# Kernel tuning notes

Hardware: AMD Instinct MI355X
Metric: run time of the kernel (lower is better)

The kernel has to match this reference:

```python
import jax, jax.numpy as jnp
import numpy as np

D_MODEL = 2048
M = 128          # compression rate
N_H = 16         # query heads
C = 128          # head dim
D_C = 512        # query compression dim
N_GROUPS = 4
D_G = 512
ROPE_DIM = 64
EPS = 1e-6
B, S = 2, 8192


def _layernorm(x, gamma, beta):
    mu = x.mean(axis=-1, keepdims=True)
    var = ((x - mu) ** 2).mean(axis=-1, keepdims=True)
    return (x - mu) * jax.lax.rsqrt(var + EPS) * gamma + beta


def _partial_rope(q):
    # q: [B,S,H,C]; rotate last ROPE_DIM dims with interleaved complex RoPE
    half = ROPE_DIM // 2
    inv_freq = 1.0 / (10000.0 ** (jnp.arange(0, ROPE_DIM, 2, dtype=jnp.float32) / ROPE_DIM))
    ang = jnp.arange(S, dtype=jnp.float32)[:, None] * inv_freq[None, :]   # [S,half]
    cos = jnp.cos(ang)[None, :, None, :]
    sin = jnp.sin(ang)[None, :, None, :]
    x_part, x_rope = q[..., : C - ROPE_DIM], q[..., C - ROPE_DIM:]
    e, o = x_rope[..., 0::2], x_rope[..., 1::2]
    re = e * cos - o * sin
    ro = e * sin + o * cos
    rot = jnp.stack([re, ro], axis=-1).reshape(*e.shape[:-1], ROPE_DIM)
    return jnp.concatenate([x_part, rot.astype(q.dtype)], axis=-1)


def setup_inputs() -> dict:
    key = jax.random.key(0)
    ks = jax.random.split(key, 12)
    std = 0.02
    inp = {
        "x": jax.random.normal(ks[0], (B, S, D_MODEL), jnp.float32),
        "w_kv": jax.random.normal(ks[1], (D_MODEL, C), jnp.float32) * std,
        "w_z": jax.random.normal(ks[2], (D_MODEL, C), jnp.float32) * std,
        "b_comp": jax.random.normal(ks[3], (M, C), jnp.float32) * std,
        "w_dq": jax.random.normal(ks[4], (D_MODEL, D_C), jnp.float32) * std,
        "w_uq": jax.random.normal(ks[5], (D_C, N_H * C), jnp.float32) * std,
        "o_down_w": jax.random.normal(ks[6], (N_GROUPS, (N_H // N_GROUPS) * C, D_G), jnp.float32) * std,
        "o_up_w": jax.random.normal(ks[7], (N_GROUPS * D_G, D_MODEL), jnp.float32) * std,
        "kv_gamma": jnp.ones((C,), jnp.float32),
        "kv_beta": jnp.zeros((C,), jnp.float32),
        "q_gamma": jnp.ones((C,), jnp.float32),
        "q_beta": jnp.zeros((C,), jnp.float32),
        "sink_logits": jnp.zeros((N_H,), jnp.float32),
    }
    return inp


def reference(x, w_kv, w_z, b_comp, w_dq, w_uq, o_down_w, o_up_w,
              kv_gamma, kv_beta, q_gamma, q_beta, sink_logits):
    n_comp = S // M
    # ---- HeavyCompressor: softmax-weighted pooling per non-overlapping block
    c_proj = x @ w_kv                                     # [B,S,C]
    z = x @ w_z                                           # [B,S,C]
    zb = z.reshape(B, n_comp, M, C) + b_comp              # [B,Nc,M,C]
    w = jax.nn.softmax(zb, axis=2)
    comp = (w * c_proj.reshape(B, n_comp, M, C)).sum(axis=2)   # [B,Nc,C]
    k_comp = _layernorm(comp, kv_gamma, kv_beta)
    v_comp = comp
    # ---- queries: low-rank down/up projection, per-head LN, partial RoPE
    q = (x @ w_dq @ w_uq).reshape(B, S, N_H, C)
    q = _layernorm(q, q_gamma, q_beta)
    q = _partial_rope(q)
    # ---- dense attention over compressed KV with sink-logit denominator
    scores = jnp.einsum("bshc,bkc->bhsk", q.astype(jnp.float32),
                        k_comp.astype(jnp.float32)) / (C ** 0.5)
    allowed = jnp.arange(S)[:, None] >= jnp.arange(n_comp)[None, :] * M  # [S,Nc]
    p = jnp.where(allowed[None, None], jnp.exp(scores), 0.0)
    sink = jnp.exp(sink_logits).reshape(1, N_H, 1, 1)
    attn = p / (p.sum(axis=-1, keepdims=True) + sink)
    out = jnp.einsum("bhsk,bkc->bshc", attn.astype(x.dtype),
                     v_comp.astype(jnp.float32)).astype(x.dtype)
    # ---- grouped output projection
    gsz = N_H // N_GROUPS
    out_g = out.reshape(B, S, N_GROUPS, gsz * C)
    down = jnp.einsum("bsgi,gio->bsgo", out_g, o_down_w).reshape(B, S, N_GROUPS * D_G)
    return down @ o_up_w                                  # [B,S,D_MODEL]
```

## Files before the change

### kernel.cpp

```cpp
#include <hip/hip_runtime.h>
#include <hip/hip_bf16.h>

using bf16 = __hip_bfloat16;
typedef __attribute__((ext_vector_type(8))) short bf16x8;
typedef __attribute__((ext_vector_type(4))) float f32x4;

#define DM 2048

#define OFF_WCZQ  0x00000000ULL
#define OFF_WUQ   0x00300000ULL
#define OFF_DOWNB 0x00500000ULL
#define OFF_WUP   0x00700000ULL
#define OFF_W2T   0x00F00000ULL
#define OFF_KC    0x01700000ULL
#define OFF_VT    0x01710000ULL
#define OFF_ROPE  0x01720000ULL
#define OFF_XB    0x01A00000ULL
#define OFF_CZQ   0x05A00000ULL
#define OFF_QF    0x07300000ULL

__device__ __forceinline__ void async16(const void* g, void* l) {
  __builtin_amdgcn_global_load_lds(
      (const __attribute__((address_space(1))) unsigned int*)g,
      (__attribute__((address_space(3))) unsigned int*)l, 16, 0, 0);
}

__device__ __forceinline__ f32x4 mfma16(bf16x8 a, bf16x8 b, f32x4 c) {
  return __builtin_amdgcn_mfma_f32_16x16x32_bf16(a, b, c, 0, 0, 0);
}

__device__ __forceinline__ float b2f(short u) {
  unsigned x = ((unsigned)(unsigned short)u) << 16;
  return __builtin_bit_cast(float, x);
}
__device__ __forceinline__ short f2bs(float f) {
  return __builtin_bit_cast(short, __float2bfloat16(f));
}

#define SB0 __builtin_amdgcn_sched_barrier(0)

__device__ __forceinline__ void cvt8(const float* __restrict__ in, bf16* __restrict__ out, size_t i) {
  float4 a = *(const float4*)(in + i);
  float4 b = *(const float4*)(in + i + 4);
  struct alignas(16) B8 { bf16 v[8]; } r;
  r.v[0] = __float2bfloat16(a.x); r.v[1] = __float2bfloat16(a.y);
  r.v[2] = __float2bfloat16(a.z); r.v[3] = __float2bfloat16(a.w);
  r.v[4] = __float2bfloat16(b.x); r.v[5] = __float2bfloat16(b.y);
  r.v[6] = __float2bfloat16(b.z); r.v[7] = __float2bfloat16(b.w);
  *(B8*)(out + i) = r;
}

__global__ __launch_bounds__(256) void prep_k(
    const float* __restrict__ w_kv, const float* __restrict__ w_z,
    const float* __restrict__ w_dq, const float* __restrict__ w_uq,
    const float* __restrict__ o_up, const float* __restrict__ o_down,
    const float* __restrict__ x,
    bf16* __restrict__ WCZQ, bf16* __restrict__ WUQ, bf16* __restrict__ WUP,
    bf16* __restrict__ DOWNB, bf16* __restrict__ XB, float2* __restrict__ ROPE) {
  __shared__ float t[32][33];
  const int b = blockIdx.x;
  if (b < 6656) {
    const float* src; bf16* dst; int K, N, tx, ty;
    if (b < 256)       { src = w_kv; dst = WCZQ;              K = 2048; N = 128;  int i = b;        tx = i % 4;  ty = i / 4;  }
    else if (b < 512)  { src = w_z;  dst = WCZQ + 128 * 2048; K = 2048; N = 128;  int i = b - 256;  tx = i % 4;  ty = i / 4;  }
    else if (b < 1536) { src = w_dq; dst = WCZQ + 256 * 2048; K = 2048; N = 512;  int i = b - 512;  tx = i % 16; ty = i / 16; }
    else if (b < 2560) { src = w_uq; dst = WUQ;               K = 512;  N = 2048; int i = b - 1536; tx = i % 64; ty = i / 64; }
    else               { src = o_up; dst = WUP;               K = 2048; N = 2048; int i = b - 2560; tx = i % 64; ty = i / 64; }
    const int tn0 = tx * 32, tk0 = ty * 32;
    const int lx = threadIdx.x & 31, ly = threadIdx.x >> 5;
#pragma unroll
    for (int p = 0; p < 4; p++) {
      int k = tk0 + ly + p * 8, n = tn0 + lx;
      if (k < K && n < N) t[ly + p * 8][lx] = src[(size_t)k * N + n];
    }
    __syncthreads();
#pragma unroll
    for (int p = 0; p < 4; p++) {
      int n = tn0 + ly + p * 8, k = tk0 + lx;
      if (n < N && k < K) dst[(size_t)n * K + k] = __float2bfloat16(t[lx][ly + p * 8]);
    }
  } else if (b < 7168) {
    cvt8(o_down, DOWNB, ((size_t)(b - 6656) * 256 + threadIdx.x) * 8);
  } else if (b < 8192) {
    int idx = (b - 7168) * 256 + threadIdx.x;
    int s = idx >> 5, i = idx & 31;
    double f = pow(10000.0, -((double)(2 * i)) / 64.0);
    double a = (double)s * f;
    ROPE[idx] = make_float2((float)cos(a), (float)sin(a));
  } else {
    cvt8(x, XB, ((size_t)(b - 8192) * 256 + threadIdx.x) * 8);
  }
}

template <int OUT_BF16>
__device__ __forceinline__ void gemm8p_body(
    char* ldsb,
    const bf16* __restrict__ A, int lda,
    const bf16* __restrict__ Bt, int ldb,
    void* __restrict__ Cp, int ldc, int K, int ntiles, int wgid) {
  const int tid = threadIdx.x;
  const int lane = tid & 63, wid = tid >> 6;
  const int wr = wid >> 2, wc = wid & 3;
  const int mt = wgid / ntiles, nt = wgid % ntiles;
  const int srow = tid >> 2;
  const int sunit = (tid & 3) ^ ((tid >> 3) & 3);
  const bf16* gA = A + (size_t)(mt * 256 + srow) * lda + (sunit << 3);
  const bf16* gB = Bt + (size_t)(nt * 256 + srow) * ldb + (sunit << 3);
  char* ldsA = ldsb + tid * 16;
  char* ldsB = ldsb + 32768 + tid * 16;

#define STAGE_A(dd, h, kc) async16(gA + (kc) + (h) * 32, ldsA + (dd) * 65536 + (h) * 16384)
#define STAGE_B(dd, h, kc) async16(gB + (kc) + (h) * 32, ldsB + (dd) * 65536 + (h) * 16384)

  const int l15 = lane & 15, g = lane >> 4;
  const int gsw = g ^ ((l15 >> 1) & 3);
  const char* ardb = ldsb + (size_t)(wr * 64 + l15) * 64 + (gsw << 4);
  const char* brdb = ldsb + 32768 + (size_t)(wc * 64 + l15) * 64 + (gsw << 4);

  f32x4 acc[4][4] = {};
  STAGE_A(0, 0, 0); STAGE_B(0, 0, 0); STAGE_A(0, 1, 0); STAGE_B(0, 1, 0);

  const int nkt = K >> 6;
  for (int t = 0; t < nkt; ++t) {
    const int d = t & 1;
    const char* aB = ardb + d * 65536;
    const char* bB = brdb + d * 65536;
    const int kn = (t + 1) << 6;
    const bool pf = (t + 1) < nkt;
    bf16x8 a[4], b0, b1;
    SB0;
    asm volatile("s_waitcnt vmcnt(2)" ::: "memory");
    __builtin_amdgcn_s_barrier();
    asm volatile("" ::: "memory");
    SB0;
    if (pf) STAGE_A(d ^ 1, 0, kn);
#pragma unroll
    for (int m = 0; m < 4; m++) a[m] = *(const bf16x8*)(aB + m * 1024);
    b0 = *(const bf16x8*)(bB);
    b1 = *(const bf16x8*)(bB + 1024);
    __builtin_amdgcn_s_setprio(1);
#pragma unroll
    for (int m = 0; m < 4; m++) {
      acc[m][0] = mfma16(a[m], b0, acc[m][0]);
      acc[m][1] = mfma16(a[m], b1, acc[m][1]);
    }
    __builtin_amdgcn_s_setprio(0);
    if (pf) STAGE_B(d ^ 1, 0, kn);
    b0 = *(const bf16x8*)(bB + 2048);
    b1 = *(const bf16x8*)(bB + 3072);
    __builtin_amdgcn_s_setprio(1);
#pragma unroll
    for (int m = 0; m < 4; m++) {
      acc[m][2] = mfma16(a[m], b0, acc[m][2]);
      acc[m][3] = mfma16(a[m], b1, acc[m][3]);
    }
    __builtin_amdgcn_s_setprio(0);
    SB0;
    if (pf) asm volatile("s_waitcnt vmcnt(2)" ::: "memory");
    else    asm volatile("s_waitcnt vmcnt(0)" ::: "memory");
    __builtin_amdgcn_s_barrier();
    asm volatile("" ::: "memory");
    SB0;
    if (pf) STAGE_A(d ^ 1, 1, kn);
#pragma unroll
    for (int m = 0; m < 4; m++) a[m] = *(const bf16x8*)(aB + 16384 + m * 1024);
    b0 = *(const bf16x8*)(bB + 16384);
    b1 = *(const bf16x8*)(bB + 16384 + 1024);
    __builtin_amdgcn_s_setprio(1);
#pragma unroll
    for (int m = 0; m < 4; m++) {
      acc[m][0] = mfma16(a[m], b0, acc[m][0]);
      acc[m][1] = mfma16(a[m], b1, acc[m][1]);
    }
    __builtin_amdgcn_s_setprio(0);
    if (pf) STAGE_B(d ^ 1, 1, kn);
    b0 = *(const bf16x8*)(bB + 16384 + 2048);
    b1 = *(const bf16x8*)(bB + 16384 + 3072);
    __builtin_amdgcn_s_setprio(1);
#pragma unroll
    for (int m = 0; m < 4; m++) {
      acc[m][2] = mfma16(a[m], b0, acc[m][2]);
      acc[m][3] = mfma16(a[m], b1, acc[m][3]);
    }
    __builtin_amdgcn_s_setprio(0);
  }
#undef STAGE_A
#undef STAGE_B

  const int r4 = (lane >> 4) << 2;
  const size_t row0 = (size_t)mt * 256 + wr * 64;
  const int col0 = nt * 256 + wc * 64;
#pragma unroll
  for (int m = 0; m < 4; m++)
#pragma unroll
    for (int n = 0; n < 4; n++)
#pragma unroll
      for (int j = 0; j < 4; j++) {
        size_t row = row0 + m * 16 + r4 + j;
        size_t col = (size_t)col0 + n * 16 + l15;
        if (OUT_BF16) ((bf16*)Cp)[row * ldc + col] = __float2bfloat16(acc[m][n][j]);
        else          ((float*)Cp)[row * ldc + col] = acc[m][n][j];
      }
}

template <int OUT_BF16>
__global__ __launch_bounds__(1024, 1) void gemm8p(
    const bf16* __restrict__ A, int lda,
    const bf16* __restrict__ Bt, int ldb,
    void* __restrict__ Cp, int ldc, int K, int ntiles) {
  __shared__ __align__(16) char lds[131072];
  const int wgid = (blockIdx.x & 7) * (gridDim.x >> 3) + (blockIdx.x >> 3);
  gemm8p_body<OUT_BF16>(lds, A, lda, Bt, ldb, Cp, ldc, K, ntiles, wgid);
}

__global__ __launch_bounds__(1024, 1) void czq_w2t_k(
    const bf16* __restrict__ XB, const bf16* __restrict__ WCZQ, bf16* __restrict__ CZQ,
    const bf16* __restrict__ WUP, const bf16* __restrict__ DOWNB, bf16* __restrict__ W2T,
    const float* __restrict__ b_comp, const float* __restrict__ kv_g,
    const float* __restrict__ kv_b, bf16* __restrict__ KC, bf16* __restrict__ VT) {
  __shared__ __align__(16) char lds[131072];
  const int bx = blockIdx.x;
  if (bx < 192) {
    const int wgid = (bx & 7) * 24 + (bx >> 3);
    gemm8p_body<1>(lds, XB, DM, WCZQ, DM, CZQ, 768, DM, 3, wgid);
    const int mt = wgid / 3, nt = wgid % 3;
    if (nt == 0) {
      asm volatile("s_waitcnt vmcnt(0)" ::: "memory");
      __syncthreads();
      float* sm = (float*)lds;
      const int t = threadIdx.x;
      const int local = t >> 9;
      const int tt = t & 511;
      const int c = tt & 127, qtr = tt >> 7;
      const int blk = 2 * mt + local;
      const size_t t0 = (size_t)blk * 128;
      float num = 0.f, den = 0.f;
      for (int m = qtr * 32; m < qtr * 32 + 32; m++) {
        const bf16* r = CZQ + (t0 + m) * 768;
        float w = expf(__bfloat162float(r[128 + c]) + b_comp[m * 128 + c]);
        den += w;
        num += w * __bfloat162float(r[c]);
      }
      float* sn = sm + local * 1152;
      float* sd = sm + local * 1152 + 512;
      float* sv = sm + local * 1152 + 1024;
      sn[qtr * 128 + c] = num;
      sd[qtr * 128 + c] = den;
      __syncthreads();
      if (qtr == 0)
        sv[c] = (sn[c] + sn[128 + c] + sn[256 + c] + sn[384 + c]) /
                (sd[c] + sd[128 + c] + sd[256 + c] + sd[384 + c]);
      __syncthreads();
      if (qtr == 0) {
        float v = sv[c];
        float mu = 0.f;
        for (int i = 0; i < 128; i++) mu += sv[i];
        mu *= (1.f / 128.f);
        float var = 0.f;
        for (int i = 0; i < 128; i++) { float d = sv[i] - mu; var += d * d; }
        var *= (1.f / 128.f);
        float kc = (v - mu) * rsqrtf(var + 1e-6f) * kv_g[c] + kv_b[c];
        const int bb = blk >> 6, kb = blk & 63;
        KC[(size_t)blk * 128 + c] = __float2bfloat16(kc);
        VT[(size_t)bb * 8192 + c * 64 + kb] = __float2bfloat16(v);
      }
    }
  } else {
    const int b2 = bx - 192;
    const int grp = b2 >> 4, inner = b2 & 15;
    const int wgid = (inner & 7) * 2 + (inner >> 3);
    gemm8p_body<1>(lds, WUP + grp * 512, DM, DOWNB + (size_t)grp * 512 * 512, 512,
                   W2T + grp * 512, DM, 512, 2, wgid);
  }
}

__global__ __launch_bounds__(256) void attn_k(
    const bf16* __restrict__ qln, const bf16* __restrict__ kc,
    const bf16* __restrict__ vt, const float* __restrict__ sink_logits,
    const float* __restrict__ gamma, const float* __restrict__ beta,
    const float2* __restrict__ rope, bf16* __restrict__ out) {
  __shared__ bf16 Qs[128 * 128];
  const int qt = blockIdx.x, hh = blockIdx.y, b = blockIdx.z;
  const int nk = qt + 1;
  const int ntk = (nk + 15) >> 4;
  const int nkk = (nk + 31) >> 5;
  const int tid = threadIdx.x, wave = tid >> 6, lane = tid & 63;
  const int l15 = lane & 15, g = lane >> 4;
  const size_t t0 = (size_t)b * 8192 + (size_t)qt * 128;
  const bf16* kbase = kc + (size_t)b * 64 * 128;
  const bf16* vbase = vt + (size_t)b * 128 * 64;

  {
    const int q = tid >> 1, hf = tid & 1;
    const bf16* gq = qln + (t0 + q) * 2048 + hh * 128 + hf * 64;
    bf16x8 r[8];
#pragma unroll
    for (int i = 0; i < 8; i++) r[i] = *(const bf16x8*)(gq + i * 8);
    float sum = 0.f;
#pragma unroll
    for (int i = 0; i < 8; i++)
#pragma unroll
      for (int j = 0; j < 8; j++) sum += b2f(r[i][j]);
    sum += __shfl_xor(sum, 1);
    const float mu = sum * (1.f / 128.f);
    float var = 0.f;
#pragma unroll
    for (int i = 0; i < 8; i++)
#pragma unroll
      for (int j = 0; j < 8; j++) { float d = b2f(r[i][j]) - mu; var += d * d; }
    var += __shfl_xor(var, 1);
    const float inv = rsqrtf(var * (1.f / 128.f) + 1e-6f);
    const int c0 = hf * 64;
#pragma unroll
    for (int i = 0; i < 8; i++) {
      float y[8];
#pragma unroll
      for (int j = 0; j < 8; j++) {
        int ch = c0 + i * 8 + j;
        y[j] = (b2f(r[i][j]) - mu) * inv * gamma[ch] + beta[ch];
      }
      if (hf) {
#pragma unroll
        for (int j = 0; j < 8; j += 2) {
          float2 cs = rope[((size_t)qt * 128 + q) * 32 + i * 4 + (j >> 1)];
          float e = y[j], o = y[j + 1];
          y[j] = e * cs.x - o * cs.y;
          y[j + 1] = e * cs.y + o * cs.x;
        }
      }
      bf16x8 w;
#pragma unroll
      for (int j = 0; j < 8; j++) w[j] = f2bs(y[j]);
      *(bf16x8*)(Qs + q * 128 + ((hf * 8 + (i ^ (q & 7))) << 3)) = w;
    }
  }
  __syncthreads();

  bf16x8 af[2][4];
#pragma unroll
  for (int m = 0; m < 2; m++) {
    const int q = wave * 32 + m * 16 + l15;
#pragma unroll
    for (int kk = 0; kk < 4; kk++) {
      const int u = (kk * 4 + g) ^ (q & 7);
      af[m][kk] = *(const bf16x8*)(Qs + q * 128 + u * 8);
    }
  }
  __syncthreads();

  f32x4 sacc[2][4] = {};
#pragma unroll
  for (int n = 0; n < 4; n++) {
    if (n < ntk) {
      const bf16* kr = kbase + (n * 16 + l15) * 128 + g * 8;
      bf16x8 b0 = *(const bf16x8*)(kr);
      bf16x8 b1 = *(const bf16x8*)(kr + 32);
      bf16x8 b2 = *(const bf16x8*)(kr + 64);
      bf16x8 b3 = *(const bf16x8*)(kr + 96);
      __builtin_amdgcn_s_setprio(1);
      sacc[0][n] = mfma16(af[0][0], b0, sacc[0][n]);
      sacc[1][n] = mfma16(af[1][0], b0, sacc[1][n]);
      sacc[0][n] = mfma16(af[0][1], b1, sacc[0][n]);
      sacc[1][n] = mfma16(af[1][1], b1, sacc[1][n]);
      sacc[0][n] = mfma16(af[0][2], b2, sacc[0][n]);
      sacc[1][n] = mfma16(af[1][2], b2, sacc[1][n]);
      sacc[0][n] = mfma16(af[0][3], b3, sacc[0][n]);
      sacc[1][n] = mfma16(af[1][3], b3, sacc[1][n]);
      __builtin_amdgcn_s_setprio(0);
    }
  }

  const float sink = expf(sink_logits[hh]);
  const float scale = 0.088388347648318447f;
  bf16* P = Qs;
#pragma unroll
  for (int m = 0; m < 2; m++) {
    float pv[4][4];
    float rs[4] = {0.f, 0.f, 0.f, 0.f};
#pragma unroll
    for (int n = 0; n < 4; n++) {
      int key = n * 16 + l15;
#pragma unroll
      for (int j = 0; j < 4; j++) {
        float p = (key < nk) ? expf(sacc[m][n][j] * scale) : 0.f;
        pv[n][j] = p;
        rs[j] += p;
      }
    }
#pragma unroll
    for (int j = 0; j < 4; j++) {
      float v = rs[j];
      v += __shfl_xor(v, 1); v += __shfl_xor(v, 2);
      v += __shfl_xor(v, 4); v += __shfl_xor(v, 8);
      rs[j] = 1.0f / (v + sink);
    }
    const int row0 = wave * 32 + m * 16 + (g << 2);
#pragma unroll
    for (int n = 0; n < 4; n++)
#pragma unroll
      for (int j = 0; j < 4; j++) {
        int q = row0 + j;
        int k = n * 16 + l15;
        P[q * 64 + ((((k >> 3) ^ (q & 7)) << 3) | (k & 7))] =
            __float2bfloat16(pv[n][j] * rs[j]);
      }
  }

  f32x4 oacc[2][8] = {};
#pragma unroll
  for (int kk = 0; kk < 2; kk++) {
    if (kk < nkk) {
      bf16x8 pa[2];
#pragma unroll
      for (int m = 0; m < 2; m++) {
        const int q = wave * 32 + m * 16 + l15;
        const int u = (kk * 4 + g) ^ (q & 7);
        pa[m] = *(const bf16x8*)(P + q * 64 + u * 8);
      }
#pragma unroll
      for (int n = 0; n < 8; n++) {
        bf16x8 vb = *(const bf16x8*)(vbase + (n * 16 + l15) * 64 + kk * 32 + g * 8);
        __builtin_amdgcn_s_setprio(1);
        oacc[0][n] = mfma16(pa[0], vb, oacc[0][n]);
        oacc[1][n] = mfma16(pa[1], vb, oacc[1][n]);
        __builtin_amdgcn_s_setprio(0);
      }
    }
  }

  bf16* ob = out + t0 * 2048 + hh * 128;
  const int r4 = g << 2;
#pragma unroll
  for (int m = 0; m < 2; m++)
#pragma unroll
    for (int n = 0; n < 8; n++)
#pragma unroll
      for (int j = 0; j < 4; j++)
        ob[(size_t)(wave * 32 + m * 16 + r4 + j) * 2048 + n * 16 + l15] =
            __float2bfloat16(oacc[m][n][j]);
}

extern "C" void kernel_launch(void* const* d_in, const int* in_sizes, int n_in,
                              void* d_out, int out_size, void* d_ws, size_t ws_size,
                              hipStream_t stream) {
  const float* x      = (const float*)d_in[0];
  const float* w_kv   = (const float*)d_in[1];
  const float* w_z    = (const float*)d_in[2];
  const float* b_comp = (const float*)d_in[3];
  const float* w_dq   = (const float*)d_in[4];
  const float* w_uq   = (const float*)d_in[5];
  const float* o_down = (const float*)d_in[6];
  const float* o_up   = (const float*)d_in[7];
  const float* kv_g   = (const float*)d_in[8];
  const float* kv_b   = (const float*)d_in[9];
  const float* q_g    = (const float*)d_in[10];
  const float* q_b    = (const float*)d_in[11];
  const float* sinkl  = (const float*)d_in[12];
  char* ws = (char*)d_ws;
  bf16*   WCZQ  = (bf16*)(ws + OFF_WCZQ);
  bf16*   WUQ   = (bf16*)(ws + OFF_WUQ);
  bf16*   DOWNB = (bf16*)(ws + OFF_DOWNB);
  bf16*   WUP   = (bf16*)(ws + OFF_WUP);
  bf16*   W2T   = (bf16*)(ws + OFF_W2T);
  bf16*   KC    = (bf16*)(ws + OFF_KC);
  bf16*   VT    = (bf16*)(ws + OFF_VT);
  float2* ROPE  = (float2*)(ws + OFF_ROPE);
  bf16*   XB    = (bf16*)(ws + OFF_XB);
  bf16*   CZQ   = (bf16*)(ws + OFF_CZQ);
  bf16*   QF    = (bf16*)(ws + OFF_QF);
  bf16*   ATT   = (bf16*)(ws + OFF_XB);
  float*  OUT   = (float*)d_out;

  prep_k<<<24576, 256, 0, stream>>>(w_kv, w_z, w_dq, w_uq, o_up, o_down, x,
                                    WCZQ, WUQ, WUP, DOWNB, XB, ROPE);
  czq_w2t_k<<<256, 1024, 0, stream>>>(XB, WCZQ, CZQ, WUP, DOWNB, W2T,
                                      b_comp, kv_g, kv_b, KC, VT);
  gemm8p<1><<<512, 1024, 0, stream>>>(CZQ + 256, 768, WUQ, 512, QF, DM, 512, 8);
  attn_k<<<dim3(64, 16, 2), 256, 0, stream>>>(QF, KC, VT, sinkl, q_g, q_b, ROPE, ATT);
  gemm8p<0><<<512, 1024, 0, stream>>>(ATT, DM, W2T, DM, OUT, DM, DM, 8);
}
```

Before: 362.2 us.

## Fuse query up-projection GEMM into attention kernel via LDS-resident Q tiles

The query up-projection GEMM now writes its 256x256 bf16 output tile into LDS instead of global memory. The same 1024-thread workgroup then runs four 256-thread attention sub-blocks, each on a 128x128 (token, head) slice read from LDS. This removes a kernel launch and the global write and read of the full Q tensor (32 MB bf16). In exchange, attention runs at one workgroup per CU with 1024 threads, so occupancy and latency hiding may suffer compared with the separate 256-thread attention kernel.

```diff
diff --git a/kernel.cpp b/kernel.cpp
--- a/kernel.cpp
+++ b/kernel.cpp
@@ -17,7 +17,6 @@
 #define OFF_ROPE  0x01720000ULL
 #define OFF_XB    0x01A00000ULL
 #define OFF_CZQ   0x05A00000ULL
-#define OFF_QF    0x07300000ULL
 
 __device__ __forceinline__ void async16(const void* g, void* l) {
   __builtin_amdgcn_global_load_lds(
@@ -92,7 +91,7 @@
   }
 }
 
-template <int OUT_BF16>
+template <int OUT_MODE>
 __device__ __forceinline__ void gemm8p_body(
     char* ldsb,
     const bf16* __restrict__ A, int lda,
@@ -188,29 +187,45 @@
 #undef STAGE_B
 
   const int r4 = (lane >> 4) << 2;
-  const size_t row0 = (size_t)mt * 256 + wr * 64;
-  const int col0 = nt * 256 + wc * 64;
-#pragma unroll
-  for (int m = 0; m < 4; m++)
-#pragma unroll
-    for (int n = 0; n < 4; n++)
-#pragma unroll
-      for (int j = 0; j < 4; j++) {
-        size_t row = row0 + m * 16 + r4 + j;
-        size_t col = (size_t)col0 + n * 16 + l15;
-        if (OUT_BF16) ((bf16*)Cp)[row * ldc + col] = __float2bfloat16(acc[m][n][j]);
-        else          ((float*)Cp)[row * ldc + col] = acc[m][n][j];
-      }
-}
-
-template <int OUT_BF16>
+  if (OUT_MODE == 2) {
+    __syncthreads();
+    bf16* q16 = (bf16*)ldsb;
+#pragma unroll
+    for (int m = 0; m < 4; m++)
+#pragma unroll
+      for (int n = 0; n < 4; n++)
+#pragma unroll
+        for (int j = 0; j < 4; j++) {
+          int rl = wr * 64 + m * 16 + r4 + j;
+          int cl = wc * 64 + n * 16 + l15;
+          int s = ((rl >> 7) << 1) | (cl >> 7);
+          q16[s * 16384 + (rl & 127) * 128 + (cl & 127)] = __float2bfloat16(acc[m][n][j]);
+        }
+  } else {
+    const size_t row0 = (size_t)mt * 256 + wr * 64;
+    const int col0 = nt * 256 + wc * 64;
+#pragma unroll
+    for (int m = 0; m < 4; m++)
+#pragma unroll
+      for (int n = 0; n < 4; n++)
+#pragma unroll
+        for (int j = 0; j < 4; j++) {
+          size_t row = row0 + m * 16 + r4 + j;
+          size_t col = (size_t)col0 + n * 16 + l15;
+          if (OUT_MODE == 1) ((bf16*)Cp)[row * ldc + col] = __float2bfloat16(acc[m][n][j]);
+          else               ((float*)Cp)[row * ldc + col] = acc[m][n][j];
+        }
+  }
+}
+
+template <int OUT_MODE>
 __global__ __launch_bounds__(1024, 1) void gemm8p(
     const bf16* __restrict__ A, int lda,
     const bf16* __restrict__ Bt, int ldb,
     void* __restrict__ Cp, int ldc, int K, int ntiles) {
   __shared__ __align__(16) char lds[131072];
   const int wgid = (blockIdx.x & 7) * (gridDim.x >> 3) + (blockIdx.x >> 3);
-  gemm8p_body<OUT_BF16>(lds, A, lda, Bt, ldb, Cp, ldc, K, ntiles, wgid);
+  gemm8p_body<OUT_MODE>(lds, A, lda, Bt, ldb, Cp, ldc, K, ntiles, wgid);
 }
 
 __global__ __launch_bounds__(1024, 1) void czq_w2t_k(
@@ -274,28 +289,39 @@
   }
 }
 
-__global__ __launch_bounds__(256) void attn_k(
-    const bf16* __restrict__ qln, const bf16* __restrict__ kc,
-    const bf16* __restrict__ vt, const float* __restrict__ sink_logits,
+__global__ __launch_bounds__(1024, 1) void qup_attn_k(
+    const bf16* __restrict__ QMID, const bf16* __restrict__ WUQ,
+    const bf16* __restrict__ kc, const bf16* __restrict__ vt,
+    const float* __restrict__ sink_logits,
     const float* __restrict__ gamma, const float* __restrict__ beta,
     const float2* __restrict__ rope, bf16* __restrict__ out) {
-  __shared__ bf16 Qs[128 * 128];
-  const int qt = blockIdx.x, hh = blockIdx.y, b = blockIdx.z;
+  __shared__ __align__(16) char lds[131072];
+  const int wgid = (blockIdx.x & 7) * 64 + (blockIdx.x >> 3);
+  gemm8p_body<2>(lds, QMID, 768, WUQ, 512, nullptr, 0, 512, 8, wgid);
+  __syncthreads();
+
+  const int mt = wgid >> 3, nt = wgid & 7;
+  const int sub = threadIdx.x >> 8;
+  const int lt = threadIdx.x & 255;
+  const int lw = (threadIdx.x >> 6) & 3;
+  const int lane = threadIdx.x & 63;
+  const int l15 = lane & 15, g = lane >> 4;
+  const int tglob0 = mt * 256 + (sub >> 1) * 128;
+  const int b = tglob0 >> 13;
+  const int qt = (tglob0 & 8191) >> 7;
+  const int hh = nt * 2 + (sub & 1);
   const int nk = qt + 1;
   const int ntk = (nk + 15) >> 4;
   const int nkk = (nk + 31) >> 5;
-  const int tid = threadIdx.x, wave = tid >> 6, lane = tid & 63;
-  const int l15 = lane & 15, g = lane >> 4;
-  const size_t t0 = (size_t)b * 8192 + (size_t)qt * 128;
+  bf16* Qs = (bf16*)lds + sub * 16384;
   const bf16* kbase = kc + (size_t)b * 64 * 128;
   const bf16* vbase = vt + (size_t)b * 128 * 64;
 
   {
-    const int q = tid >> 1, hf = tid & 1;
-    const bf16* gq = qln + (t0 + q) * 2048 + hh * 128 + hf * 64;
+    const int q = lt >> 1, hf = lt & 1;
     bf16x8 r[8];
 #pragma unroll
-    for (int i = 0; i < 8; i++) r[i] = *(const bf16x8*)(gq + i * 8);
+    for (int i = 0; i < 8; i++) r[i] = *(const bf16x8*)(Qs + q * 128 + hf * 64 + i * 8);
     float sum = 0.f;
 #pragma unroll
     for (int i = 0; i < 8; i++)
@@ -339,7 +365,7 @@
   bf16x8 af[2][4];
 #pragma unroll
   for (int m = 0; m < 2; m++) {
-    const int q = wave * 32 + m * 16 + l15;
+    const int q = lw * 32 + m * 16 + l15;
 #pragma unroll
     for (int kk = 0; kk < 4; kk++) {
       const int u = (kk * 4 + g) ^ (q & 7);
@@ -394,7 +420,7 @@
       v += __shfl_xor(v, 4); v += __shfl_xor(v, 8);
       rs[j] = 1.0f / (v + sink);
     }
-    const int row0 = wave * 32 + m * 16 + (g << 2);
+    const int row0 = lw * 32 + m * 16 + (g << 2);
 #pragma unroll
     for (int n = 0; n < 4; n++)
 #pragma unroll
@@ -413,7 +439,7 @@
       bf16x8 pa[2];
 #pragma unroll
       for (int m = 0; m < 2; m++) {
-        const int q = wave * 32 + m * 16 + l15;
+        const int q = lw * 32 + m * 16 + l15;
         const int u = (kk * 4 + g) ^ (q & 7);
         pa[m] = *(const bf16x8*)(P + q * 64 + u * 8);
       }
@@ -428,7 +454,7 @@
     }
   }
 
-  bf16* ob = out + t0 * 2048 + hh * 128;
+  bf16* ob = out + ((size_t)b * 8192 + (size_t)qt * 128) * 2048 + hh * 128;
   const int r4 = g << 2;
 #pragma unroll
   for (int m = 0; m < 2; m++)
@@ -436,7 +462,7 @@
     for (int n = 0; n < 8; n++)
 #pragma unroll
       for (int j = 0; j < 4; j++)
-        ob[(size_t)(wave * 32 + m * 16 + r4 + j) * 2048 + n * 16 + l15] =
+        ob[(size_t)(lw * 32 + m * 16 + r4 + j) * 2048 + n * 16 + l15] =
             __float2bfloat16(oacc[m][n][j]);
 }
 
@@ -467,7 +493,6 @@
   float2* ROPE  = (float2*)(ws + OFF_ROPE);
   bf16*   XB    = (bf16*)(ws + OFF_XB);
   bf16*   CZQ   = (bf16*)(ws + OFF_CZQ);
-  bf16*   QF    = (bf16*)(ws + OFF_QF);
   bf16*   ATT   = (bf16*)(ws + OFF_XB);
   float*  OUT   = (float*)d_out;
 
@@ -475,7 +500,7 @@
                                     WCZQ, WUQ, WUP, DOWNB, XB, ROPE);
   czq_w2t_k<<<256, 1024, 0, stream>>>(XB, WCZQ, CZQ, WUP, DOWNB, W2T,
                                       b_comp, kv_g, kv_b, KC, VT);
-  gemm8p<1><<<512, 1024, 0, stream>>>(CZQ + 256, 768, WUQ, 512, QF, DM, 512, 8);
-  attn_k<<<dim3(64, 16, 2), 256, 0, stream>>>(QF, KC, VT, sinkl, q_g, q_b, ROPE, ATT);
+  qup_attn_k<<<512, 1024, 0, stream>>>(CZQ + 256, WUQ, KC, VT, sinkl,
+                                       q_g, q_b, ROPE, ATT);
   gemm8p<0><<<512, 1024, 0, stream>>>(ATT, DM, W2T, DM, OUT, DM, DM, 8);
 }
```

Measured after the change: 338.1 us. -6.6%, faster.
